# Performance work log

Measured on AMD Instinct MI355X. Metric: run time of the kernel, lower is better.

The kernel has to match this reference:

```python
import jax, jax.numpy as jnp
import numpy as np

N_HEADS = 32
N_KV = 16
HEAD_DIM = 128
REPEATS = N_HEADS // N_KV
ROPE_THETA = 10000.0
SOFTCAP = 50.0
SCALE = 1.0 / np.sqrt(144.0)


def _rope_cos_sin(L, dtype):
    half = HEAD_DIM // 2
    inv_freq = 1.0 / (ROPE_THETA ** (jnp.arange(0, HEAD_DIM, 2, dtype=jnp.float32) / HEAD_DIM))
    ang = jnp.arange(L, dtype=jnp.float32)[:, None] * inv_freq[None, :]  # [L, half]
    return jnp.cos(ang).astype(dtype), jnp.sin(ang).astype(dtype)


def _apply_rope(t, cos, sin):
    # t: [B, H, L, D]; non-traditional (rotate-half) RoPE
    half = HEAD_DIM // 2
    t1, t2 = t[..., :half], t[..., half:]
    c = cos[None, None, :, :]
    s = sin[None, None, :, :]
    return jnp.concatenate([t1 * c - t2 * s, t2 * c + t1 * s], axis=-1)


def setup_inputs() -> dict:
    key = jax.random.key(0)
    k1, k2, k3, k4, k5 = jax.random.split(key, 5)
    B, L, D = 1, 2048, 4608
    x = jax.random.normal(k1, (B, L, D), dtype=jnp.float32)
    wq = jax.random.normal(k2, (N_HEADS * HEAD_DIM, D), dtype=jnp.float32) * 0.02
    wk = jax.random.normal(k3, (N_KV * HEAD_DIM, D), dtype=jnp.float32) * 0.02
    wv = jax.random.normal(k4, (N_KV * HEAD_DIM, D), dtype=jnp.float32) * 0.02
    wo = jax.random.normal(k5, (D, N_HEADS * HEAD_DIM), dtype=jnp.float32) * 0.02
    mask = jnp.tril(jnp.ones((L, L), dtype=bool))  # causal
    return {"x": x, "mask": mask, "wq": wq, "wk": wk, "wv": wv, "wo": wo}


def reference(x, mask, wq, wk, wv, wo):
    B, L, D = x.shape
    q = (x @ wq.T).reshape(B, L, N_HEADS, HEAD_DIM).transpose(0, 2, 1, 3)
    k = (x @ wk.T).reshape(B, L, N_KV, HEAD_DIM).transpose(0, 2, 1, 3)
    v = (x @ wv.T).reshape(B, L, N_KV, HEAD_DIM).transpose(0, 2, 1, 3)

    cos, sin = _rope_cos_sin(L, x.dtype)
    q = _apply_rope(q, cos, sin) * jnp.asarray(SCALE, x.dtype)
    k = _apply_rope(k, cos, sin)

    # GQA: group queries per kv head -> [B, n_kv, repeats, L, D]
    qg = q.reshape(B, N_KV, REPEATS, L, HEAD_DIM)
    scores = jnp.einsum("bgrqd,bgkd->bgrqk", qg, k)
    scores = jnp.tanh(scores / SOFTCAP) * SOFTCAP
    neg = jnp.asarray(jnp.finfo(scores.dtype).min, scores.dtype)
    scores = jnp.where(mask[None, None, None, :, :], scores, neg)
    probs = jax.nn.softmax(scores, axis=-1)
    out = jnp.einsum("bgrqk,bgkd->bgrqd", probs, v)  # [B, n_kv, rep, L, D]
    out = out.reshape(B, N_HEADS, L, HEAD_DIM).transpose(0, 2, 1, 3).reshape(B, L, -1)
    return out @ wo.T
```

## Files before the change

kernel.cpp:

```cpp
#include <hip/hip_runtime.h>
#include <hip/hip_bf16.h>
#include <math.h>

typedef unsigned short u16;
typedef __attribute__((ext_vector_type(8))) short s16x8;
typedef __attribute__((ext_vector_type(4))) float f32x4;

#define SCALE 0.083333333333333329f
#define SOFTCAP_INV 0.02f
#define LDO 4128

__device__ __forceinline__ u16 f2bf(float f) {
    unsigned u = __float_as_uint(f);
    unsigned r = 0x7fffu + ((u >> 16) & 1u);
    return (u16)((u + r) >> 16);
}
__device__ __forceinline__ float bf2f(u16 v) {
    return __uint_as_float(((unsigned)v) << 16);
}

__device__ __forceinline__ float fast_tanh(float x) {
    float e = __expf(2.0f * x);
    return 1.0f - 2.0f / (e + 1.0f);
}

__global__ __launch_bounds__(256) void cast_kernel(const float* __restrict__ in,
                                                   u16* __restrict__ out) {
    size_t i = ((size_t)blockIdx.x * 256 + threadIdx.x) * 4;
    float4 v = *(const float4*)(in + i);
    ushort4 o;
    o.x = f2bf(v.x); o.y = f2bf(v.y); o.z = f2bf(v.z); o.w = f2bf(v.w);
    *(ushort4*)(out + i) = o;
}

__global__ __launch_bounds__(256) void cast_pad_kernel(const float* __restrict__ in,
                                                       u16* __restrict__ out) {
    size_t i = ((size_t)blockIdx.x * 256 + threadIdx.x) * 4;
    size_t row = i >> 12;
    int col = (int)(i & 4095);
    float4 v = *(const float4*)(in + i);
    ushort4 o;
    o.x = f2bf(v.x); o.y = f2bf(v.y); o.z = f2bf(v.z); o.w = f2bf(v.w);
    *(ushort4*)(out + row * LDO + col) = o;
}

__global__ __launch_bounds__(256) void rope_table_kernel(float* __restrict__ cosT,
                                                         float* __restrict__ sinT) {
    int idx = blockIdx.x * 256 + threadIdx.x;
    int i = idx & 63, pos = idx >> 6;
    float inv = __expf(-((float)i / 64.0f) * 9.210340371976184f);
    float ang = (float)pos * inv;
    cosT[idx] = cosf(ang);
    sinT[idx] = sinf(ang);
}

__global__ __launch_bounds__(256) void rope_q_kernel(const u16* __restrict__ T16,
                                                     u16* __restrict__ Qb,
                                                     const float* __restrict__ cosT,
                                                     const float* __restrict__ sinT) {
    int idx = blockIdx.x * 256 + threadIdx.x;
    int i = idx & 63;
    int head = (idx >> 6) & 31;
    int pos = idx >> 11;
    size_t rbase = (size_t)pos * 8192 + head * 128 + i;
    float t1 = bf2f(T16[rbase]), t2 = bf2f(T16[rbase + 64]);
    float c = cosT[(pos << 6) + i], s = sinT[(pos << 6) + i];
    size_t wbase = (size_t)pos * 4096 + head * 128 + i;
    Qb[wbase]      = f2bf((t1 * c - t2 * s) * SCALE);
    Qb[wbase + 64] = f2bf((t2 * c + t1 * s) * SCALE);
}

__global__ __launch_bounds__(256) void rope_k_kernel(const u16* __restrict__ T16,
                                                     u16* __restrict__ Kb,
                                                     const float* __restrict__ cosT,
                                                     const float* __restrict__ sinT) {
    int idx = blockIdx.x * 256 + threadIdx.x;
    int i = idx & 63;
    int head = (idx >> 6) & 15;
    int pos = idx >> 10;
    size_t rbase = (size_t)pos * 8192 + 4096 + head * 128 + i;
    float t1 = bf2f(T16[rbase]), t2 = bf2f(T16[rbase + 64]);
    float c = cosT[(pos << 6) + i], s = sinT[(pos << 6) + i];
    size_t wbase = (size_t)pos * 2048 + head * 128 + i;
    Kb[wbase]      = f2bf(t1 * c - t2 * s);
    Kb[wbase + 64] = f2bf(t2 * c + t1 * s);
}

__global__ __launch_bounds__(256) void vtrans_kernel(const u16* __restrict__ T16,
                                                     u16* __restrict__ Vt) {
    __shared__ u16 tile[32][33];
    int bc = (blockIdx.x & 63) << 5;
    int bl = (blockIdx.x >> 6) << 5;
    int x = threadIdx.x & 31, y = threadIdx.x >> 5;
    #pragma unroll
    for (int yy = y; yy < 32; yy += 8)
        tile[yy][x] = T16[(size_t)(bl + yy) * 8192 + 6144 + bc + x];
    __syncthreads();
    #pragma unroll
    for (int yy = y; yy < 32; yy += 8)
        Vt[(size_t)(bc + yy) * 2048 + bl + x] = tile[x][yy];
}

#define STAGE_A(buf, ktt, l)                                                            \
    __builtin_amdgcn_global_load_lds(                                                   \
        (const __attribute__((address_space(1))) unsigned int*)(aSrc + (size_t)(ktt) * 64 + (size_t)(l) * 64 * lda), \
        (__attribute__((address_space(3))) unsigned int*)(&lds[buf][0][(l) * 4096 + ldsoff]), 16, 0, 0)
#define STAGE_B(buf, ktt, l)                                                            \
    __builtin_amdgcn_global_load_lds(                                                   \
        (const __attribute__((address_space(1))) unsigned int*)(bSrc + (size_t)(ktt) * 64 + (size_t)(l) * 64 * ldb), \
        (__attribute__((address_space(3))) unsigned int*)(&lds[buf][1][(l) * 4096 + ldsoff]), 16, 0, 0)

template<bool OUT_BF16>
__device__ __forceinline__ void gemm256_core(const u16* __restrict__ A,
                                             const u16* __restrict__ B,
                                             void* __restrict__ C,
                                             int N, int K, int lda, int ldb,
                                             int bm, int bn,
                                             u16 (&lds)[2][2][16384]) {
    int t = threadIdx.x;
    int lane = t & 63, wave = t >> 6;
    int wm = wave >> 2, wn = wave & 3;
    int fr = lane & 15, fq = lane >> 4;
    int sw = (fr & 7) << 4;

    int srow = wave * 8 + (lane >> 3);
    int scb = ((lane & 7) * 16) ^ (((lane >> 3) & 7) << 4);
    const u16* aSrc = A + (size_t)(bm * 256 + srow) * lda + (scb >> 1);
    const u16* bSrc = B + (size_t)(bn * 256 + srow) * ldb + (scb >> 1);
    int ldsoff = wave * 512;

    f32x4 acc[8][4];
    #pragma unroll
    for (int m = 0; m < 8; m++)
        #pragma unroll
        for (int n = 0; n < 4; n++)
            acc[m][n] = (f32x4){0.f, 0.f, 0.f, 0.f};

    STAGE_B(0, 0, 0); STAGE_B(0, 0, 1); STAGE_B(0, 0, 2); STAGE_B(0, 0, 3);
    STAGE_A(0, 0, 0); STAGE_A(0, 0, 2); STAGE_A(0, 0, 1); STAGE_A(0, 0, 3);

    int nt = K >> 6;
    for (int it = 0; it < nt; ++it) {
        int cur = it & 1, nxt = cur ^ 1;
        bool more = (it + 1 < nt);
        const char* Ab = (const char*)&lds[cur][0][0];
        const char* Bb = (const char*)&lds[cur][1][0];
        int cb0 = (fq * 16) ^ sw;
        int cb1 = (64 + fq * 16) ^ sw;

        if (more) {
            STAGE_B(nxt, it + 1, 0); STAGE_B(nxt, it + 1, 1);
            __builtin_amdgcn_sched_barrier(0);
            asm volatile("s_waitcnt vmcnt(4)" ::: "memory");
        } else {
            asm volatile("s_waitcnt vmcnt(2)" ::: "memory");
        }
        __builtin_amdgcn_s_barrier();
        s16x8 b0[4], a0[4];
        #pragma unroll
        for (int n = 0; n < 4; ++n)
            b0[n] = *(const s16x8*)(Bb + (wn * 64 + n * 16 + fr) * 128 + cb0);
        #pragma unroll
        for (int m = 0; m < 4; ++m)
            a0[m] = *(const s16x8*)(Ab + (wm * 128 + m * 16 + fr) * 128 + cb0);
        __builtin_amdgcn_s_setprio(1);
        #pragma unroll
        for (int m = 0; m < 4; ++m)
            #pragma unroll
            for (int n = 0; n < 4; ++n)
                acc[m][n] = __builtin_amdgcn_mfma_f32_16x16x32_bf16(a0[m], b0[n], acc[m][n], 0, 0, 0);
        __builtin_amdgcn_s_setprio(0);
        __builtin_amdgcn_s_barrier();

        if (more) {
            STAGE_B(nxt, it + 1, 2); STAGE_B(nxt, it + 1, 3);
            __builtin_amdgcn_sched_barrier(0);
            asm volatile("s_waitcnt vmcnt(4)" ::: "memory");
        } else {
            asm volatile("s_waitcnt vmcnt(0)" ::: "memory");
        }
        __builtin_amdgcn_s_barrier();
        s16x8 a1[4];
        #pragma unroll
        for (int m = 0; m < 4; ++m)
            a1[m] = *(const s16x8*)(Ab + (wm * 128 + (4 + m) * 16 + fr) * 128 + cb0);
        __builtin_amdgcn_s_setprio(1);
        #pragma unroll
        for (int m = 0; m < 4; ++m)
            #pragma unroll
            for (int n = 0; n < 4; ++n)
                acc[4 + m][n] = __builtin_amdgcn_mfma_f32_16x16x32_bf16(a1[m], b0[n], acc[4 + m][n], 0, 0, 0);
        __builtin_amdgcn_s_setprio(0);
        __builtin_amdgcn_s_barrier();

        if (more) { STAGE_A(nxt, it + 1, 0); STAGE_A(nxt, it + 1, 2); }
        s16x8 b1[4], a2[4];
        #pragma unroll
        for (int n = 0; n < 4; ++n)
            b1[n] = *(const s16x8*)(Bb + (wn * 64 + n * 16 + fr) * 128 + cb1);
        #pragma unroll
        for (int m = 0; m < 4; ++m)
            a2[m] = *(const s16x8*)(Ab + (wm * 128 + m * 16 + fr) * 128 + cb1);
        __builtin_amdgcn_s_setprio(1);
        #pragma unroll
        for (int m = 0; m < 4; ++m)
            #pragma unroll
            for (int n = 0; n < 4; ++n)
                acc[m][n] = __builtin_amdgcn_mfma_f32_16x16x32_bf16(a2[m], b1[n], acc[m][n], 0, 0, 0);
        __builtin_amdgcn_s_setprio(0);
        __builtin_amdgcn_s_barrier();

        if (more) { STAGE_A(nxt, it + 1, 1); STAGE_A(nxt, it + 1, 3); }
        s16x8 a3[4];
        #pragma unroll
        for (int m = 0; m < 4; ++m)
            a3[m] = *(const s16x8*)(Ab + (wm * 128 + (4 + m) * 16 + fr) * 128 + cb1);
        __builtin_amdgcn_s_setprio(1);
        #pragma unroll
        for (int m = 0; m < 4; ++m)
            #pragma unroll
            for (int n = 0; n < 4; ++n)
                acc[4 + m][n] = __builtin_amdgcn_mfma_f32_16x16x32_bf16(a3[m], b1[n], acc[4 + m][n], 0, 0, 0);
        __builtin_amdgcn_s_setprio(0);
        __builtin_amdgcn_s_barrier();
    }

    #pragma unroll
    for (int m = 0; m < 8; ++m) {
        int row = bm * 256 + wm * 128 + m * 16 + fq * 4;
        #pragma unroll
        for (int n = 0; n < 4; ++n) {
            int col = bn * 256 + wn * 64 + n * 16 + fr;
            #pragma unroll
            for (int r = 0; r < 4; ++r) {
                if (OUT_BF16) ((u16*)C)[(size_t)(row + r) * N + col] = f2bf(acc[m][n][r]);
                else          ((float*)C)[(size_t)(row + r) * N + col] = acc[m][n][r];
            }
        }
    }
}

__global__ __launch_bounds__(512) void gemm256_qkv(const u16* __restrict__ A,
                                                   const u16* __restrict__ B,
                                                   u16* __restrict__ C, int K) {
    __shared__ u16 lds[2][2][16384];
    int bid = blockIdx.x;
    int x = bid & 7, j = bid >> 3;
    int bn = x * 4 + (j & 3);
    int bm = j >> 2;
    gemm256_core<true>(A, B, C, 8192, K, K, K, bm, bn, lds);
}

__global__ __launch_bounds__(512) void gemm256_out(const u16* __restrict__ A,
                                                   const u16* __restrict__ B,
                                                   float* __restrict__ C, int K) {
    __shared__ u16 lds[2][2][16384];
    int bid = blockIdx.x;
    int j = (bid & 7) * 18 + (bid >> 3);
    int bm = j & 7;
    int bn = j >> 3;
    gemm256_core<false>(A, B, C, 4608, K, LDO, LDO, bm, bn, lds);
}

__global__ __launch_bounds__(256) void attn_kernel(const u16* __restrict__ Qb,
                                                   const u16* __restrict__ Kb,
                                                   const u16* __restrict__ Vt,
                                                   u16* __restrict__ Ob) {
    __shared__ u16 Ks[64 * 128];
    __shared__ u16 Vs[128 * 64];
    __shared__ u16 Pst[4 * 1024];

    int bid = blockIdx.x;
    int hq = bid & 31;
    int qb = 31 - (bid >> 5);
    int g = hq >> 1;
    int t = threadIdx.x;
    int lane = t & 63, wave = t >> 6;
    int fr = lane & 15, fq = lane >> 4;
    int sw = (fr & 7) << 4;
    int qrow0 = qb * 64 + wave * 16;
    u16* Pw = &Pst[wave * 1024];

    s16x8 qf[4];
    #pragma unroll
    for (int s = 0; s < 4; s++)
        qf[s] = *(const s16x8*)&Qb[(size_t)(qrow0 + fr) * 4096 + hq * 128 + s * 32 + fq * 8];

    f32x4 o[8];
    #pragma unroll
    for (int c = 0; c < 8; c++) o[c] = (f32x4){0.f, 0.f, 0.f, 0.f};
    float mi[4] = {-INFINITY, -INFINITY, -INFINITY, -INFINITY};
    float li[4] = {0.f, 0.f, 0.f, 0.f};

    int w4 = wave * 4;
    int nT = qb + 1;
    for (int kt = 0; kt < nT; kt++) {
        int kv0 = kt << 6;
        __syncthreads();
        #pragma unroll
        for (int i = 0; i < 4; i++) {
            int li_ = w4 + i;
            int rk = li_ * 4 + (lane >> 4);
            int cbk = ((lane & 15) * 16) ^ ((rk & 7) << 4);
            const u16* srcK = Kb + (size_t)(kv0 + rk) * 2048 + g * 128 + (cbk >> 1);
            __builtin_amdgcn_global_load_lds(
                (const __attribute__((address_space(1))) unsigned int*)srcK,
                (__attribute__((address_space(3))) unsigned int*)(Ks + li_ * 512), 16, 0, 0);
            int rv = li_ * 8 + (lane >> 3);
            int cbv = ((lane & 7) * 16) ^ ((rv & 7) << 4);
            const u16* srcV = Vt + (size_t)(g * 128 + rv) * 2048 + kv0 + (cbv >> 1);
            __builtin_amdgcn_global_load_lds(
                (const __attribute__((address_space(1))) unsigned int*)srcV,
                (__attribute__((address_space(3))) unsigned int*)(Vs + li_ * 512), 16, 0, 0);
        }
        __syncthreads();

        if (kv0 <= qrow0 + 15) {
            f32x4 sf[4];
            #pragma unroll
            for (int j = 0; j < 4; j++) sf[j] = (f32x4){0.f, 0.f, 0.f, 0.f};
            #pragma unroll
            for (int j = 0; j < 4; j++)
                #pragma unroll
                for (int s = 0; s < 4; s++) {
                    s16x8 kf = *(const s16x8*)&Ks[(j * 16 + fr) * 128 + (((s * 64 + fq * 16) ^ sw) >> 1)];
                    sf[j] = __builtin_amdgcn_mfma_f32_16x16x32_bf16(qf[s], kf, sf[j], 0, 0, 0);
                }
            float pmax[4] = {-INFINITY, -INFINITY, -INFINITY, -INFINITY};
            #pragma unroll
            for (int j = 0; j < 4; j++)
                #pragma unroll
                for (int r = 0; r < 4; r++) {
                    float sc = 50.f * fast_tanh(sf[j][r] * SOFTCAP_INV);
                    int colk = kv0 + j * 16 + fr;
                    int rowq = qrow0 + fq * 4 + r;
                    sc = (colk > rowq) ? -INFINITY : sc;
                    sf[j][r] = sc;
                    pmax[r] = fmaxf(pmax[r], sc);
                }
            #pragma unroll
            for (int d = 1; d < 16; d <<= 1)
                #pragma unroll
                for (int r = 0; r < 4; r++)
                    pmax[r] = fmaxf(pmax[r], __shfl_xor(pmax[r], d));
            float al[4], psum[4] = {0.f, 0.f, 0.f, 0.f};
            #pragma unroll
            for (int r = 0; r < 4; r++) {
                float mn = fmaxf(mi[r], pmax[r]);
                al[r] = __expf(mi[r] - mn);
                mi[r] = mn;
            }
            #pragma unroll
            for (int j = 0; j < 4; j++)
                #pragma unroll
                for (int r = 0; r < 4; r++) {
                    float p = __expf(sf[j][r] - mi[r]);
                    sf[j][r] = p;
                    psum[r] += p;
                }
            #pragma unroll
            for (int d = 1; d < 16; d <<= 1)
                #pragma unroll
                for (int r = 0; r < 4; r++)
                    psum[r] += __shfl_xor(psum[r], d);
            #pragma unroll
            for (int r = 0; r < 4; r++)
                li[r] = li[r] * al[r] + psum[r];
            #pragma unroll
            for (int c = 0; c < 8; c++)
                #pragma unroll
                for (int r = 0; r < 4; r++)
                    o[c][r] *= al[r];
            #pragma unroll
            for (int j = 0; j < 4; j++)
                #pragma unroll
                for (int r = 0; r < 4; r++) {
                    int row = fq * 4 + r, col = j * 16 + fr;
                    int byteoff = (row * 128 + col * 2) ^ ((row & 7) << 4);
                    *(u16*)((char*)Pw + byteoff) = f2bf(sf[j][r]);
                }
            #pragma unroll
            for (int s = 0; s < 2; s++) {
                int rbyte = (fr * 128 + s * 64 + fq * 16) ^ sw;
                s16x8 pf = *(const s16x8*)((const char*)Pw + rbyte);
                #pragma unroll
                for (int c = 0; c < 8; c++) {
                    s16x8 vf = *(const s16x8*)&Vs[(c * 16 + fr) * 64 + (((s * 64 + fq * 16) ^ sw) >> 1)];
                    o[c] = __builtin_amdgcn_mfma_f32_16x16x32_bf16(pf, vf, o[c], 0, 0, 0);
                }
            }
        }
    }
    #pragma unroll
    for (int c = 0; c < 8; c++)
        #pragma unroll
        for (int r = 0; r < 4; r++) {
            int rowq = qrow0 + fq * 4 + r;
            Ob[(size_t)rowq * LDO + hq * 128 + c * 16 + fr] = f2bf(o[c][r] / li[r]);
        }
}

extern "C" void kernel_launch(void* const* d_in, const int* in_sizes, int n_in,
                              void* d_out, int out_size, void* d_ws, size_t ws_size,
                              hipStream_t stream) {
    const float* x  = (const float*)d_in[0];
    const float* wq = (const float*)d_in[2];
    const float* wk = (const float*)d_in[3];
    const float* wv = (const float*)d_in[4];
    const float* wo = (const float*)d_in[5];
    float* out = (float*)d_out;

    char* w = (char*)d_ws;
    u16*   xb   = (u16*)(w);
    u16*   wb   = (u16*)(w + 18874368);
    u16*   T16  = (u16*)(w + 94371840);
    u16*   Ob   = (u16*)(w + 127926272);
    u16*   Qbuf = (u16*)(w + 144834560);
    u16*   Kbuf = (u16*)(w + 161611776);
    u16*   Vt   = (u16*)(w + 170000384);
    float* cosT = (float*)(w + 178388992);
    float* sinT = (float*)(w + 178913280);

    rope_table_kernel<<<512, 256, 0, stream>>>(cosT, sinT);
    cast_kernel<<<9216, 256, 0, stream>>>(x, xb);

    cast_kernel<<<18432, 256, 0, stream>>>(wq, wb);
    cast_kernel<<<9216, 256, 0, stream>>>(wk, wb + (size_t)4096 * 4608);
    cast_kernel<<<9216, 256, 0, stream>>>(wv, wb + (size_t)6144 * 4608);

    gemm256_qkv<<<256, 512, 0, stream>>>(xb, wb, T16, 4608);

    rope_q_kernel<<<16384, 256, 0, stream>>>(T16, Qbuf, cosT, sinT);
    rope_k_kernel<<<8192, 256, 0, stream>>>(T16, Kbuf, cosT, sinT);
    vtrans_kernel<<<4096, 256, 0, stream>>>(T16, Vt);

    attn_kernel<<<1024, 256, 0, stream>>>(Qbuf, Kbuf, Vt, Ob);

    cast_pad_kernel<<<18432, 256, 0, stream>>>(wo, wb);
    gemm256_out<<<144, 512, 0, stream>>>(Ob, wb, out, 4096);
}
```

Baseline: 468.0 us.

## Replace online softmax with fixed-max exponent using softcap score bound

The tanh softcap bounds every score to at most 50, so the attention kernel now uses 50 as a fixed row maximum. It computes p = exp(-100/(e+1)) directly with exp2/rcp intrinsics. This removes the running max, the cross-lane max and sum shuffles per tile, and the per-tile rescaling of the output accumulators. Row sums are kept per lane and reduced once at the end. The risk is underflow: if every score in a row sits near the lower bound of -50, p approaches exp(-100), which can flush to zero and leave the row sum at zero.

```diff
diff --git a/kernel.cpp b/kernel.cpp
--- a/kernel.cpp
+++ b/kernel.cpp
@@ -7,7 +7,6 @@
 typedef __attribute__((ext_vector_type(4))) float f32x4;
 
 #define SCALE 0.083333333333333329f
-#define SOFTCAP_INV 0.02f
 #define LDO 4128
 
 __device__ __forceinline__ u16 f2bf(float f) {
@@ -17,11 +16,6 @@
 }
 __device__ __forceinline__ float bf2f(u16 v) {
     return __uint_as_float(((unsigned)v) << 16);
-}
-
-__device__ __forceinline__ float fast_tanh(float x) {
-    float e = __expf(2.0f * x);
-    return 1.0f - 2.0f / (e + 1.0f);
 }
 
 __global__ __launch_bounds__(256) void cast_kernel(const float* __restrict__ in,
@@ -289,8 +283,7 @@
     f32x4 o[8];
     #pragma unroll
     for (int c = 0; c < 8; c++) o[c] = (f32x4){0.f, 0.f, 0.f, 0.f};
-    float mi[4] = {-INFINITY, -INFINITY, -INFINITY, -INFINITY};
-    float li[4] = {0.f, 0.f, 0.f, 0.f};
+    float liacc[4] = {0.f, 0.f, 0.f, 0.f};
 
     int w4 = wave * 4;
     int nT = qb + 1;
@@ -326,51 +319,19 @@
                     s16x8 kf = *(const s16x8*)&Ks[(j * 16 + fr) * 128 + (((s * 64 + fq * 16) ^ sw) >> 1)];
                     sf[j] = __builtin_amdgcn_mfma_f32_16x16x32_bf16(qf[s], kf, sf[j], 0, 0, 0);
                 }
-            float pmax[4] = {-INFINITY, -INFINITY, -INFINITY, -INFINITY};
             #pragma unroll
             for (int j = 0; j < 4; j++)
                 #pragma unroll
                 for (int r = 0; r < 4; r++) {
-                    float sc = 50.f * fast_tanh(sf[j][r] * SOFTCAP_INV);
+                    float s_ = sf[j][r];
+                    float e = __builtin_amdgcn_exp2f(s_ * 0.05770780163f);
+                    float p = __builtin_amdgcn_exp2f(-144.2695041f * __builtin_amdgcn_rcpf(e + 1.0f));
                     int colk = kv0 + j * 16 + fr;
                     int rowq = qrow0 + fq * 4 + r;
-                    sc = (colk > rowq) ? -INFINITY : sc;
-                    sf[j][r] = sc;
-                    pmax[r] = fmaxf(pmax[r], sc);
+                    p = (colk > rowq) ? 0.0f : p;
+                    sf[j][r] = p;
+                    liacc[r] += p;
                 }
-            #pragma unroll
-            for (int d = 1; d < 16; d <<= 1)
-                #pragma unroll
-                for (int r = 0; r < 4; r++)
-                    pmax[r] = fmaxf(pmax[r], __shfl_xor(pmax[r], d));
-            float al[4], psum[4] = {0.f, 0.f, 0.f, 0.f};
-            #pragma unroll
-            for (int r = 0; r < 4; r++) {
-                float mn = fmaxf(mi[r], pmax[r]);
-                al[r] = __expf(mi[r] - mn);
-                mi[r] = mn;
-            }
-            #pragma unroll
-            for (int j = 0; j < 4; j++)
-                #pragma unroll
-                for (int r = 0; r < 4; r++) {
-                    float p = __expf(sf[j][r] - mi[r]);
-                    sf[j][r] = p;
-                    psum[r] += p;
-                }
-            #pragma unroll
-            for (int d = 1; d < 16; d <<= 1)
-                #pragma unroll
-                for (int r = 0; r < 4; r++)
-                    psum[r] += __shfl_xor(psum[r], d);
-            #pragma unroll
-            for (int r = 0; r < 4; r++)
-                li[r] = li[r] * al[r] + psum[r];
-            #pragma unroll
-            for (int c = 0; c < 8; c++)
-                #pragma unroll
-                for (int r = 0; r < 4; r++)
-                    o[c][r] *= al[r];
             #pragma unroll
             for (int j = 0; j < 4; j++)
                 #pragma unroll
@@ -392,11 +353,19 @@
         }
     }
     #pragma unroll
+    for (int d = 1; d < 16; d <<= 1)
+        #pragma unroll
+        for (int r = 0; r < 4; r++)
+            liacc[r] += __shfl_xor(liacc[r], d);
+    float rli[4];
+    #pragma unroll
+    for (int r = 0; r < 4; r++) rli[r] = __builtin_amdgcn_rcpf(liacc[r]);
+    #pragma unroll
     for (int c = 0; c < 8; c++)
         #pragma unroll
         for (int r = 0; r < 4; r++) {
             int rowq = qrow0 + fq * 4 + r;
-            Ob[(size_t)rowq * LDO + hq * 128 + c * 16 + fr] = f2bf(o[c][r] / li[r]);
+            Ob[(size_t)rowq * LDO + hq * 128 + c * 16 + fr] = f2bf(o[c][r] * rli[r]);
         }
 }
 
```

Result: faster. 411.7 us (-12.0%).
